# Kernel optimization log

Measured on AMD Instinct MI355X. Metric: run time of the kernel, lower is better.

The kernel has to match this reference:

```python
import jax, jax.numpy as jnp
import numpy as np

N, D, E, P, L = 50000, 128, 800000, 9, 3
EPS = 1e-5  # torch nn.LayerNorm default eps


def _layernorm(x, g, b):
    m = jnp.mean(x, axis=-1, keepdims=True)
    v = jnp.mean((x - m) ** 2, axis=-1, keepdims=True)
    return (x - m) * jax.lax.rsqrt(v + EPS) * g + b


def _pol_transform(x, M, onehot):
    # x: (N,d), M: (P,d,d), onehot: (N,P). Equivalent to bmm(x[n] @ M[pol[n]])
    # without materializing the (N,d,d) gathered map tensor.
    return jnp.einsum('nd,np,pdk->nk', x, onehot, M)


def setup_inputs() -> dict:
    key = jax.random.key(0)
    ks = jax.random.split(key, 12)
    s = 1.0 / np.sqrt(D)  # xavier-ish scale
    f32 = jnp.float32
    return {
        'x': jax.random.normal(ks[0], (N, D), f32),
        'edge_index': jax.random.randint(ks[1], (2, E), 0, N),
        'ring_polarities': jax.random.randint(ks[2], (N,), 0, P),
        'Wr': jax.random.normal(ks[3], (L, D, D), f32) * s,          # restriction weights
        'S': jax.random.normal(ks[4], (L, P, D, D), f32) * s,        # send_maps
        'dS': jax.random.normal(ks[5], (L, P, D, D), f32) * 0.01,    # delta_send
        'R': jax.random.normal(ks[6], (L, P, D, D), f32) * s,        # receive_maps
        'dR': jax.random.normal(ks[7], (L, P, D, D), f32) * 0.01,    # delta_receive
        'res_scale': jnp.full((L,), 0.92, f32),
        'W1': jax.random.normal(ks[8], (L, D, D), f32) * s,          # update Linear 1
        'b1': jnp.zeros((L, D), f32),
        'ln_g': jnp.ones((L, D), f32),                               # update LayerNorm
        'ln_b': jnp.zeros((L, D), f32),
        'W2': jax.random.normal(ks[9], (L, D, D), f32) * s,          # update Linear 2
        'b2': jnp.zeros((L, D), f32),
        'norm_g': jnp.ones((L, D), f32),                             # output LayerNorm
        'norm_b': jnp.zeros((L, D), f32),
    }


def reference(x, edge_index, ring_polarities, Wr, S, dS, R, dR, res_scale,
              W1, b1, ln_g, ln_b, W2, b2, norm_g, norm_b):
    src, tgt = edge_index[0], edge_index[1]
    pol = ring_polarities % P
    onehot = jax.nn.one_hot(pol, P, dtype=x.dtype)  # (N,P)
    # deg is accumulated over row(=src) in the original code, then used to
    # normalize the scatter over col(=tgt) -- preserved faithfully.
    deg = jax.ops.segment_sum(jnp.ones((E,), x.dtype), src, num_segments=N)
    deg_norm = (1.0 / jnp.clip(deg, 1.0))[:, None]  # (N,1)

    residual = x
    for l in range(L):
        # send transform: map depends only on src-node polarity, so apply
        # per-node then gather (algebraically identical to per-edge bmm).
        xt = _pol_transform(x, S[l] + dS[l], onehot)          # (N,D)
        msg = xt[src] @ Wr[l].T                               # (E,D) restriction per edge
        agg = jax.ops.segment_sum(msg, tgt, num_segments=N)   # index_add scatter
        # receive transform depends only on tgt polarity; linear, so it
        # commutes with the sum over incoming edges.
        out = _pol_transform(agg, R[l] + dR[l], onehot) * deg_norm
        # update MLP (dropout inactive in eval)
        h = jax.nn.relu(_layernorm(out @ W1[l].T + b1[l], ln_g[l], ln_b[l]))
        out = h @ W2[l].T + b2[l]
        out = res_scale[l] * out + x                           # in==out residual
        x = _layernorm(out, norm_g[l], norm_b[l])
    return x + residual  # stack-level residual (res_proj is None, dims match)
```

## Files before the change

kernel.cpp:

```cpp
#include <hip/hip_runtime.h>
#include <hip/hip_bf16.h>

constexpr int N_ = 50000;
constexpr int D_ = 128;
constexpr int E_ = 800000;
constexpr int P_ = 9;
constexpr int L_ = 3;
constexpr float EPS_ = 1e-5f;

constexpr int TM = 64;
constexpr int CHUNK = 4096;
constexpr int NBK = (E_ + CHUNK - 1) / CHUNK;
constexpr int NBUK = 196;
constexpr int HHALF = 256 * NBK;
constexpr int HTOT = 2 * HHALF;
constexpr int NSB = HTOT / 1024;
constexpr int MAT = L_ * P_;

typedef short bf16x8 __attribute__((ext_vector_type(8)));
typedef float f32x4 __attribute__((ext_vector_type(4)));

#define GLD16(gp, lp)                                                        \
    __builtin_amdgcn_global_load_lds(                                        \
        (const __attribute__((address_space(1))) unsigned int*)(gp),         \
        (__attribute__((address_space(3))) unsigned int*)(lp), 16, 0, 0)

__device__ inline unsigned short f2bf(float f) {
    __hip_bfloat16 h = __float2bfloat16(f);
    return *reinterpret_cast<unsigned short*>(&h);
}
__device__ inline float bflo(unsigned u) { return __uint_as_float(u << 16); }
__device__ inline float bfhi(unsigned u) { return __uint_as_float(u & 0xffff0000u); }
__device__ inline float bf2f(unsigned short h) {
    return __uint_as_float((unsigned)h << 16);
}


__global__ __launch_bounds__(256) void setup_nk(const int* __restrict__ ring,
                                                int* __restrict__ pol,
                                                int* __restrict__ bcnt,
                                                const int* __restrict__ ei,
                                                int* __restrict__ histG) {
    __shared__ int h[P_];
    __shared__ int hT[256], hS[256];
    int blk = blockIdx.x, tid = threadIdx.x;
    if (tid < P_) h[tid] = 0;
    hT[tid] = 0;
    hS[tid] = 0;
    __syncthreads();
    int n = blk * 256 + tid;
    if (n < N_) {
        int p = ring[n] % P_;
        pol[n] = p;
        atomicAdd(&h[p], 1);
    }
    int base = blk * CHUNK;
#pragma unroll
    for (int i = 0; i < CHUNK / 256; ++i) {
        int e = base + tid + i * 256;
        if (e < E_) {
            atomicAdd(&hS[ei[e] >> 8], 1);
            atomicAdd(&hT[ei[E_ + e] >> 8], 1);
        }
    }
    __syncthreads();
    if (tid < P_ && h[tid] > 0) atomicAdd(&bcnt[tid], h[tid]);
    histG[tid * NBK + blk] = hT[tid];
    histG[HHALF + tid * NBK + blk] = hS[tid];
}


__global__ __launch_bounds__(1024) void scanH1(int* __restrict__ a,
                                               int* __restrict__ blkSum) {
    __shared__ int wsum[16];
    int tid = threadIdx.x, lane = tid & 63, wid = tid >> 6;
    int idx = blockIdx.x * 1024 + tid;
    int v = a[idx];
    int inc = v;
#pragma unroll
    for (int o = 1; o < 64; o <<= 1) {
        int t = __shfl_up(inc, o, 64);
        if (lane >= o) inc += t;
    }
    if (lane == 63) wsum[wid] = inc;
    __syncthreads();
    if (tid < 16) {
        int s = wsum[tid];
#pragma unroll
        for (int o = 1; o < 16; o <<= 1) {
            int t = __shfl_up(s, o, 64);
            if (tid >= o) s += t;
        }
        wsum[tid] = s;
    }
    __syncthreads();
    int wexcl = (wid == 0) ? 0 : wsum[wid - 1];
    a[idx] = wexcl + inc - v;
    if (tid == 1023) blkSum[blockIdx.x] = wsum[15];
}

__global__ void scanH2(const int* __restrict__ blkSum, int* __restrict__ blkOff,
                       int* __restrict__ offT, const int* __restrict__ bcnt,
                       int* __restrict__ boff, int* __restrict__ tileOff) {
    if (threadIdx.x != 0) return;
    int run = 0;
    for (int i = 0; i < NSB; ++i) {
        blkOff[i] = run;
        run += blkSum[i];
    }
    offT[N_] = E_;
    boff[0] = 0;
    tileOff[0] = 0;
    for (int p = 0; p < P_; ++p) {
        boff[p + 1] = boff[p] + bcnt[p];
        tileOff[p + 1] = tileOff[p] + (bcnt[p] + TM - 1) / TM;
    }
}

__global__ __launch_bounds__(1024) void scanH3(int* __restrict__ a,
                                               const int* __restrict__ blkOff) {
    int idx = blockIdx.x * 1024 + threadIdx.x;
    a[idx] += blkOff[blockIdx.x];
}


__global__ __launch_bounds__(256) void scatterTS(const int* __restrict__ ei,
                                                 const int* __restrict__ histG,
                                                 unsigned* __restrict__ bufT,
                                                 unsigned char* __restrict__ bufS8) {
    __shared__ int ldsT[256], ldsS[256];
    int blk = blockIdx.x, tid = threadIdx.x;
    ldsT[tid] = histG[tid * NBK + blk];
    ldsS[tid] = histG[HHALF + tid * NBK + blk] - E_;
    __syncthreads();
    int base = blk * CHUNK;
#pragma unroll
    for (int i = 0; i < CHUNK / 256; ++i) {
        int e = base + tid + i * 256;
        if (e < E_) {
            int s = ei[e], t = ei[E_ + e];
            int pT = atomicAdd(&ldsT[t >> 8], 1);
            bufT[pT] = ((unsigned)t << 16) | (unsigned)s;
            int pS = atomicAdd(&ldsS[s >> 8], 1);
            bufS8[pS] = (unsigned char)(s & 255);
        }
    }
}


__global__ __launch_bounds__(256) void finalize3(
    const unsigned* __restrict__ bufT, const unsigned char* __restrict__ bufS8,
    const int* __restrict__ histG, int* __restrict__ offT,
    unsigned short* __restrict__ eSrc, float* __restrict__ dnorm,
    const int* __restrict__ pol, const int* __restrict__ boff,
    int* __restrict__ bcur, int* __restrict__ blist) {
    __shared__ int s0[256];
    __shared__ int s1[256];
    int bb = blockIdx.x, tid = threadIdx.x;

    if (bb < NBUK) {
        int b = bb;
        int start = histG[b * NBK];
        int end = histG[(b + 1) * NBK];
        s0[tid] = 0;
        __syncthreads();
        for (int i = start + tid; i < end; i += 256)
            atomicAdd(&s0[(bufT[i] >> 16) & 255], 1);
        __syncthreads();
        if (tid < 64) {
            int b0 = 4 * tid;
            int v0 = s0[b0], v1 = s0[b0 + 1], v2 = s0[b0 + 2], v3 = s0[b0 + 3];
            int lsum = v0 + v1 + v2 + v3;
            int inc = lsum;
#pragma unroll
            for (int o = 1; o < 64; o <<= 1) {
                int t = __shfl_up(inc, o, 64);
                if (tid >= o) inc += t;
            }
            int excl = inc - lsum;
            s1[b0] = excl;
            s1[b0 + 1] = excl + v0;
            s1[b0 + 2] = excl + v0 + v1;
            s1[b0 + 3] = excl + v0 + v1 + v2;
        }
        __syncthreads();
        int node = (b << 8) + tid;
        if (node < N_) offT[node] = start + s1[tid];
// ... 89 lines not shown
        } else if (idx < SZ2) {
            j = idx - SZ1;
            v = W1[j];
            oh = W1h; ol = W1l;
        } else {
            j = idx - SZ2;
            int l = j >> 14, rem = j & 16383;
            int d = rem >> 7, i = rem & 127;
            v = Wr[(l << 14) + i * 128 + d];
            oh = Wrth; ol = Wrtl;
        }
        unsigned short h = f2bf(v);
        oh[j] = h;
        ol[j] = f2bf(v - bf2f(h));
    }
}


template <bool APM, bool BPM, bool OUT_SPLIT>
__global__ __launch_bounds__(256) void small_mfma(
    const unsigned short* __restrict__ Ah, const unsigned short* __restrict__ Al,
    const unsigned short* __restrict__ Bh, const unsigned short* __restrict__ Bl,
    unsigned short* __restrict__ Oh, unsigned short* __restrict__ Ol) {
    __shared__ unsigned short stg[(OUT_SPLIT ? 2 : 1) * 64 * 136];
    int tid = threadIdx.x, b = blockIdx.x;
    int mat = b >> 1, rb = b & 1;
    int l = mat / P_;
    size_t aoff = (size_t)(APM ? mat : l) * 16384 + (size_t)rb * 8192;
    size_t boff = (size_t)(BPM ? mat : l) * 16384;
    const unsigned short* ahp = Ah + aoff;
    const unsigned short* alp = Al + aoff;
    const unsigned short* bhp = Bh + boff;
    const unsigned short* blp = Bl + boff;

    int lane = tid & 63, wave = tid >> 6;
    int n = lane & 15, q = lane >> 4;
    int wr = wave * 16;

    f32x4 acc[8];
#pragma unroll
    for (int t = 0; t < 8; ++t) acc[t] = (f32x4){0.f, 0.f, 0.f, 0.f};

    int arow = (wr + n) * 128;
#pragma unroll
    for (int kc = 0; kc < 4; ++kc) {
        int ko = kc * 32 + q * 8;
        bf16x8 avh = *(const bf16x8*)(ahp + arow + ko);
        bf16x8 avl = *(const bf16x8*)(alp + arow + ko);
#pragma unroll
        for (int t = 0; t < 8; ++t) {
            int brow = (t * 16 + n) * 128;
            bf16x8 bvh = *(const bf16x8*)(bhp + brow + ko);
            bf16x8 bvl = *(const bf16x8*)(blp + brow + ko);
            acc[t] = __builtin_amdgcn_mfma_f32_16x16x32_bf16(avh, bvh, acc[t], 0, 0, 0);
            acc[t] = __builtin_amdgcn_mfma_f32_16x16x32_bf16(avh, bvl, acc[t], 0, 0, 0);
            acc[t] = __builtin_amdgcn_mfma_f32_16x16x32_bf16(avl, bvh, acc[t], 0, 0, 0);
        }
    }
#pragma unroll
    for (int t = 0; t < 8; ++t)
#pragma unroll
        for (int r = 0; r < 4; ++r) {
            int row = wr + q * 4 + r;
            float v = acc[t][r];
            unsigned short h = f2bf(v);
            stg[row * 136 + t * 16 + n] = h;
            if constexpr (OUT_SPLIT)
                stg[64 * 136 + row * 136 + t * 16 + n] = f2bf(v - bf2f(h));
        }
    __syncthreads();
    size_t obase = (size_t)mat * 16384 + (size_t)rb * 8192;
#pragma unroll
    for (int i = 0; i < 4; ++i) {
        int c = tid + i * 256;
        int r = c >> 4, off = c & 15;
        *(uint4*)(Oh + obase + r * 128 + off * 8) =
            *(const uint4*)(stg + r * 136 + off * 8);
        if constexpr (OUT_SPLIT)
            *(uint4*)(Ol + obase + r * 128 + off * 8) =
                *(const uint4*)(stg + 64 * 136 + r * 136 + off * 8);
    }
}


__device__ inline void accum_row(float* acc, uint4 r) {
    acc[0] += bflo(r.x); acc[1] += bfhi(r.x);
    acc[2] += bflo(r.y); acc[3] += bfhi(r.y);
    acc[4] += bflo(r.z); acc[5] += bfhi(r.z);
    acc[6] += bflo(r.w); acc[7] += bfhi(r.w);
}

__global__ __launch_bounds__(256) void aggregate_bf(const unsigned short* __restrict__ xt,
                                                    const int* __restrict__ offT,
                                                    const unsigned short* __restrict__ eSrc,
                                                    unsigned short* __restrict__ agg) {
    int nd = blockIdx.x * 4 + (threadIdx.x >> 6);
    if (nd >= N_) return;
    int l = threadIdx.x & 63;
    int g = l >> 4, c16 = l & 15;
    int beg = offT[nd], end = offT[nd + 1];

    float acc[8];
#pragma unroll
    for (int k = 0; k < 8; ++k) acc[k] = 0.f;

    for (int base = beg; base < end; base += 64) {
        int cnt = min(64, end - base);
        int idxv = (l < cnt) ? (int)eSrc[base + l] : 0;
        int steps = (cnt + 3) >> 2;
        int j = 0;
        for (; j + 3 < steps; j += 4) {
            int e0 = 4 * j + g, e1 = e0 + 4, e2 = e0 + 8, e3 = e0 + 12;
            int i0 = __shfl(idxv, e0, 64);
            int i1 = __shfl(idxv, e1, 64);
            int i2 = __shfl(idxv, e2, 64);
            int i3 = __shfl(idxv, e3, 64);
            int r0 = (e0 < cnt) ? i0 : N_;
            int r1 = (e1 < cnt) ? i1 : N_;
            int r2 = (e2 < cnt) ? i2 : N_;
            int r3 = (e3 < cnt) ? i3 : N_;
            uint4 v0 = ((const uint4*)(xt + (size_t)r0 * D_))[c16];
            uint4 v1 = ((const uint4*)(xt + (size_t)r1 * D_))[c16];
            uint4 v2 = ((const uint4*)(xt + (size_t)r2 * D_))[c16];
            uint4 v3 = ((const uint4*)(xt + (size_t)r3 * D_))[c16];
            accum_row(acc, v0);
            accum_row(acc, v1);
            accum_row(acc, v2);
            accum_row(acc, v3);
        }
        for (; j < steps; ++j) {
            int e0 = 4 * j + g;
            int i0 = __shfl(idxv, e0, 64);
            int r0 = (e0 < cnt) ? i0 : N_;
            uint4 v0 = ((const uint4*)(xt + (size_t)r0 * D_))[c16];
            accum_row(acc, v0);
        }
    }
#pragma unroll
    for (int k = 0; k < 8; ++k) {
        acc[k] += __shfl_xor(acc[k], 16, 64);
        acc[k] += __shfl_xor(acc[k], 32, 64);
    }
    if (g == 0) {
        uint4 o;
        o.x = (unsigned)f2bf(acc[0]) | ((unsigned)f2bf(acc[1]) << 16);
        o.y = (unsigned)f2bf(acc[2]) | ((unsigned)f2bf(acc[3]) << 16);
        o.z = (unsigned)f2bf(acc[4]) | ((unsigned)f2bf(acc[5]) << 16);
        o.w = (unsigned)f2bf(acc[6]) | ((unsigned)f2bf(acc[7]) << 16);
        ((uint4*)(agg + (size_t)nd * D_))[c16] = o;
    }
}


__device__ inline void stage_B_async(const unsigned short* __restrict__ B,
                                     unsigned short* sB, int wave, int lane) {
    int rsub = lane >> 4, cl = lane & 15;
#pragma unroll
    for (int j = 0; j < 8; ++j) {
        int seg = wave * 8 + j;
        int row = seg * 4 + rsub;
        GLD16(B + row * 128 + ((cl ^ (row & 15)) << 3), sB + seg * 512);
    }
}

__device__ inline void stage_A_async(const unsigned short* __restrict__ A,
                                     const int* rid, unsigned short* sA,
                                     int wave, int lane) {
    int rsub = lane >> 4, cl = lane & 15;
#pragma unroll
    for (int j = 0; j < 4; ++j) {
        int seg = wave * 4 + j;
        int rloc = seg * 4 + rsub;
        int rw = rid[rloc];
        size_t grow = (rw >= 0) ? (size_t)rw : (size_t)N_;
        GLD16(A + grow * 128 + ((cl ^ (rloc & 15)) << 3), sA + seg * 512);
    }
}


__global__ __launch_bounds__(256) void gemm_xt0(
    const unsigned short* __restrict__ A, const unsigned short* __restrict__ Bw,
    unsigned short* __restrict__ OutB, const int* __restrict__ blist,
    const int* __restrict__ boff, const int* __restrict__ tileOff) {
    __shared__ unsigned short sB[128 * 128];
    __shared__ unsigned short sA[64 * 128];
    __shared__ int rid[TM];
    int tid = threadIdx.x, b = blockIdx.x;
    if (b >= tileOff[P_]) return;
    int pp = 0;
    while (pp < P_ - 1 && b >= tileOff[pp + 1]) ++pp;
    int tb = b - tileOff[pp];
    int cnt = boff[pp + 1] - boff[pp];
    int nrows = min(TM, cnt - tb * TM);
    int rowbase = boff[pp] + tb * TM;

    if (tid < TM)
        rid[tid] = (tid < nrows) ? blist[rowbase + tid] : -1;
    __syncthreads();

    int lane = tid & 63, wave = tid >> 6;
    stage_B_async(Bw + (size_t)pp * D_ * D_, sB, wave, lane);
    stage_A_async(A, rid, sA, wave, lane);
    __syncthreads();

    int n = lane & 15, q = lane >> 4, wr = wave * 16;

    f32x4 acc[8];
#pragma unroll
    for (int t = 0; t < 8; ++t) acc[t] = (f32x4){0.f, 0.f, 0.f, 0.f};
#pragma unroll
    for (int kc = 0; kc < 4; ++kc) {
        int cs = (((kc << 2) + q) ^ n) << 3;
        bf16x8 af = *(const bf16x8*)(sA + (wr + n) * 128 + cs);
#pragma unroll
        for (int t = 0; t < 8; ++t) {
            bf16x8 bf = *(const bf16x8*)(sB + (t * 16 + n) * 128 + cs);
            acc[t] = __builtin_amdgcn_mfma_f32_16x16x32_bf16(af, bf, acc[t], 0, 0, 0);
        }
    }
    __syncthreads();
#pragma unroll
    for (int t = 0; t < 8; ++t)
#pragma unroll
        for (int r = 0; r < 4; ++r) {
            int rl = q * 4 + r;
            int c = ((t * 16 + n) >> 3);
            sA[(wr + rl) * 128 + ((c ^ rl) << 3) + (n & 7)] = f2bf(acc[t][r]);
        }
    __syncthreads();
#pragma unroll
    for (int i = 0; i < 4; ++i) {
        int cth = tid + i * 256;
        int r = cth >> 4, cl = cth & 15;
        int row = rid[r];
        if (row >= 0)
            *(uint4*)(OutB + (size_t)row * D_ + (cl << 3)) =
                *(const uint4*)(sA + r * 128 + ((cl ^ (r & 15)) << 3));
    }
}


template <bool LAST>
__global__ __launch_bounds__(256) void fused_layer(
    const unsigned short* __restrict__ agg, const unsigned short* __restrict__ DmAll,
    const unsigned short* __restrict__ W2b, const unsigned short* __restrict__ SnAll,
    const int* __restrict__ blist, const int* __restrict__ boff,
    const int* __restrict__ tileOff, const float* __restrict__ dnorm,
    const float* __restrict__ b1v, const float* __restrict__ g1v,
    const float* __restrict__ e1v, const float* __restrict__ b2v,
    const float* __restrict__ g2v, const float* __restrict__ e2v,
    const float* __restrict__ rs_ptr, const float* __restrict__ xres,
    const float* __restrict__ x0add, float* __restrict__ OutF,
    unsigned short* __restrict__ OutXt) {
    __shared__ unsigned short sB[128 * 128];
    __shared__ unsigned short sA[64 * 128];
    __shared__ int rid[TM];
    __shared__ float dnRow[TM];

    int tid = threadIdx.x, b = blockIdx.x;
    if (b >= tileOff[P_]) return;
    int pp = 0;
    while (pp < P_ - 1 && b >= tileOff[pp + 1]) ++pp;
    int tb = b - tileOff[pp];
    int cnt = boff[pp + 1] - boff[pp];
    int nrows = min(TM, cnt - tb * TM);
    int rowbase = boff[pp] + tb * TM;

    if (tid < TM) {
        int r = (tid < nrows) ? blist[rowbase + tid] : -1;
        rid[tid] = r;
        dnRow[tid] = (r >= 0) ? dnorm[r] : 1.f;
    }
    __syncthreads();

    int lane = tid & 63, wave = tid >> 6;
    stage_B_async(DmAll + (size_t)pp * D_ * D_, sB, wave, lane);
    stage_A_async(agg, rid, sA, wave, lane);

    int n = lane & 15, q = lane >> 4, wr = wave * 16;

    int rowid[4];
    float dn4[4];
#pragma unroll
    for (int r = 0; r < 4; ++r) {
        int rr = wr + q * 4 + r;
        rowid[r] = rid[rr];
        dn4[r] = dnRow[rr];
    }

    float xr[8][4];
#pragma unroll
    for (int t = 0; t < 8; ++t) {
        int col = t * 16 + n;
#pragma unroll
        for (int r = 0; r < 4; ++r)
            xr[t][r] = (rowid[r] >= 0) ? xres[(size_t)rowid[r] * D_ + col] : 0.f;
    }
    __syncthreads();

    f32x4 acc[8];
#pragma unroll
    for (int t = 0; t < 8; ++t) acc[t] = (f32x4){0.f, 0.f, 0.f, 0.f};
#pragma unroll
    for (int kc = 0; kc < 4; ++kc) {
        int cs = (((kc << 2) + q) ^ n) << 3;
        bf16x8 af = *(const bf16x8*)(sA + (wr + n) * 128 + cs);
#pragma unroll
        for (int t = 0; t < 8; ++t) {
            bf16x8 bf = *(const bf16x8*)(sB + (t * 16 + n) * 128 + cs);
            acc[t] = __builtin_amdgcn_mfma_f32_16x16x32_bf16(af, bf, acc[t], 0, 0, 0);
        }
    }

    {
        float rs1[4] = {0, 0, 0, 0}, rs2[4] = {0, 0, 0, 0};
#pragma unroll
        for (int t = 0; t < 8; ++t) {
            int col = t * 16 + n;
            float bia = b1v[col];
#pragma unroll
            for (int r = 0; r < 4; ++r) {
                float v = dn4[r] * acc[t][r] + bia;
                acc[t][r] = v;
                rs1[r] += v;
                rs2[r] += v * v;
            }
        }
#pragma unroll
        for (int mk = 1; mk < 16; mk <<= 1)
#pragma unroll
            for (int r = 0; r < 4; ++r) {
                rs1[r] += __shfl_xor(rs1[r], mk, 64);
                rs2[r] += __shfl_xor(rs2[r], mk, 64);
            }
        float mr[4], rv[4];
#pragma unroll
        for (int r = 0; r < 4; ++r) {
            float mm = rs1[r] * (1.f / 128.f);
            mr[r] = mm;
            rv[r] = rsqrtf(rs2[r] * (1.f / 128.f) - mm * mm + EPS_);
        }
#pragma unroll
        for (int t = 0; t < 8; ++t) {
            int col = t * 16 + n;
            float gg = g1v[col], bbv = e1v[col];
#pragma unroll
            for (int r = 0; r < 4; ++r)
                acc[t][r] = fmaxf((acc[t][r] - mr[r]) * rv[r] * gg + bbv, 0.f);
        }
    }

    __syncthreads();
    stage_B_async(W2b, sB, wave, lane);
#pragma unroll
    for (int t = 0; t < 8; ++t)
#pragma unroll
        for (int r = 0; r < 4; ++r) {
            int rl = q * 4 + r;
            int c = ((t * 16 + n) >> 3);
            sA[(wr + rl) * 128 + ((c ^ rl) << 3) + (n & 7)] = f2bf(acc[t][r]);
        }
    __syncthreads();

#pragma unroll
    for (int t = 0; t < 8; ++t) acc[t] = (f32x4){0.f, 0.f, 0.f, 0.f};
#pragma unroll
    for (int kc = 0; kc < 4; ++kc) {
        int cs = (((kc << 2) + q) ^ n) << 3;
        bf16x8 af = *(const bf16x8*)(sA + (wr + n) * 128 + cs);
#pragma unroll
        for (int t = 0; t < 8; ++t) {
            bf16x8 bf = *(const bf16x8*)(sB + (t * 16 + n) * 128 + cs);
            acc[t] = __builtin_amdgcn_mfma_f32_16x16x32_bf16(af, bf, acc[t], 0, 0, 0);
        }
    }

    {
        float rs = rs_ptr[0];
        float rs1[4] = {0, 0, 0, 0}, rs2[4] = {0, 0, 0, 0};
#pragma unroll
        for (int t = 0; t < 8; ++t) {
            int col = t * 16 + n;
            float bia = b2v[col];
#pragma unroll
            for (int r = 0; r < 4; ++r) {
                float v = rs * (acc[t][r] + bia) + xr[t][r];
                acc[t][r] = v;
                rs1[r] += v;
                rs2[r] += v * v;
            }
        }
#pragma unroll
        for (int mk = 1; mk < 16; mk <<= 1)
#pragma unroll
            for (int r = 0; r < 4; ++r) {
                rs1[r] += __shfl_xor(rs1[r], mk, 64);
                rs2[r] += __shfl_xor(rs2[r], mk, 64);
            }
        float mr[4], rv[4];
#pragma unroll
        for (int r = 0; r < 4; ++r) {
            float mm = rs1[r] * (1.f / 128.f);
            mr[r] = mm;
            rv[r] = rsqrtf(rs2[r] * (1.f / 128.f) - mm * mm + EPS_);
        }
#pragma unroll
        for (int t = 0; t < 8; ++t) {
            int col = t * 16 + n;
            float gg = g2v[col], bbv = e2v[col];
#pragma unroll
            for (int r = 0; r < 4; ++r) {
                float nv = (acc[t][r] - mr[r]) * rv[r] * gg + bbv;
                if constexpr (LAST) {
                    if (rowid[r] >= 0) nv += x0add[(size_t)rowid[r] * D_ + col];
                }
                acc[t][r] = nv;
                if (rowid[r] >= 0) OutF[(size_t)rowid[r] * D_ + col] = nv;
            }
        }
    }

    if constexpr (!LAST) {
        __syncthreads();
        stage_B_async(SnAll + (size_t)pp * D_ * D_, sB, wave, lane);
#pragma unroll
        for (int t = 0; t < 8; ++t)
#pragma unroll
            for (int r = 0; r < 4; ++r) {
                int rl = q * 4 + r;
                int c = ((t * 16 + n) >> 3);
                sA[(wr + rl) * 128 + ((c ^ rl) << 3) + (n & 7)] = f2bf(acc[t][r]);
            }
        __syncthreads();

#pragma unroll
        for (int t = 0; t < 8; ++t) acc[t] = (f32x4){0.f, 0.f, 0.f, 0.f};
#pragma unroll
        for (int kc = 0; kc < 4; ++kc) {
            int cs = (((kc << 2) + q) ^ n) << 3;
            bf16x8 af = *(const bf16x8*)(sA + (wr + n) * 128 + cs);
#pragma unroll
            for (int t = 0; t < 8; ++t) {
                bf16x8 bf = *(const bf16x8*)(sB + (t * 16 + n) * 128 + cs);
                acc[t] = __builtin_amdgcn_mfma_f32_16x16x32_bf16(af, bf, acc[t], 0, 0, 0);
            }
        }
#pragma unroll
        for (int t = 0; t < 8; ++t)
#pragma unroll
            for (int r = 0; r < 4; ++r) {
                int rl = q * 4 + r;
                int c = ((t * 16 + n) >> 3);
                sA[(wr + rl) * 128 + ((c ^ rl) << 3) + (n & 7)] = f2bf(acc[t][r]);
            }
        __syncthreads();
#pragma unroll
        for (int i = 0; i < 4; ++i) {
            int cth = tid + i * 256;
            int r = cth >> 4, cl = cth & 15;
            int row = rid[r];
            if (row >= 0)
                *(uint4*)(OutXt + (size_t)row * D_ + (cl << 3)) =
                    *(const uint4*)(sA + r * 128 + ((cl ^ (r & 15)) << 3));
        }
    }
}


extern "C" void kernel_launch(void* const* d_in, const int* in_sizes, int n_in,
                              void* d_out, int out_size, void* d_ws, size_t ws_size,
                              hipStream_t stream) {
    const float* x0 = (const float*)d_in[0];
    const int* ei = (const int*)d_in[1];
    const int* ring = (const int*)d_in[2];
    const float* Wr = (const float*)d_in[3];
    const float* S = (const float*)d_in[4];
    const float* dS = (const float*)d_in[5];
    const float* R = (const float*)d_in[6];
    const float* dR = (const float*)d_in[7];
    const float* rsc = (const float*)d_in[8];
    const float* W1 = (const float*)d_in[9];
    const float* b1 = (const float*)d_in[10];
    const float* lng = (const float*)d_in[11];
    const float* lnb = (const float*)d_in[12];
    const float* W2 = (const float*)d_in[13];
    const float* b2 = (const float*)d_in[14];
    const float* ng = (const float*)d_in[15];
    const float* nb = (const float*)d_in[16];
    float* out = (float*)d_out;

    char* w = (char*)d_ws;
    auto alloc = [&](size_t bytes) {
        char* p = w;
        w += (bytes + 15) & ~(size_t)15;
        return p;
    };
    unsigned short* xb = (unsigned short*)alloc((size_t)(N_ + 1) * D_ * 2);
    unsigned short* bufAb = (unsigned short*)alloc((size_t)(N_ + 1) * D_ * 2);
    unsigned short* bufBb = (unsigned short*)alloc((size_t)(N_ + 1) * D_ * 2);
    float* xbuf = (float*)alloc((size_t)N_ * D_ * 4);
    unsigned short* Sb = (unsigned short*)alloc((size_t)L_ * P_ * D_ * D_ * 2);
    unsigned short* Dmb = (unsigned short*)alloc((size_t)L_ * P_ * D_ * D_ * 2);
    unsigned short* W2b = (unsigned short*)alloc((size_t)L_ * D_ * D_ * 2);
    unsigned short* Arh = (unsigned short*)alloc((size_t)MAT * 16384 * 2);
    unsigned short* Arl = (unsigned short*)alloc((size_t)MAT * 16384 * 2);
    unsigned short* W1h = (unsigned short*)alloc((size_t)3 * 16384 * 2);
    unsigned short* W1l = (unsigned short*)alloc((size_t)3 * 16384 * 2);
    unsigned short* Wrth = (unsigned short*)alloc((size_t)3 * 16384 * 2);
    unsigned short* Wrtl = (unsigned short*)alloc((size_t)3 * 16384 * 2);
    unsigned short* T1th = (unsigned short*)alloc((size_t)MAT * 16384 * 2);
    unsigned short* T1tl = (unsigned short*)alloc((size_t)MAT * 16384 * 2);
    float* dnorm = (float*)alloc((size_t)N_ * 4);
    int* histG = (int*)alloc((size_t)HTOT * 4);
    unsigned* bufT = (unsigned*)alloc((size_t)E_ * 4);
    unsigned char* bufS8 = (unsigned char*)alloc((size_t)E_);
    unsigned short* eSrc = (unsigned short*)alloc((size_t)E_ * 2);
    int* offT = (int*)alloc((size_t)(N_ + 1) * 4);
    int* pol = (int*)alloc((size_t)N_ * 4);
    int* boff = (int*)alloc((size_t)(P_ + 1) * 4);
    int* tileOff = (int*)alloc((size_t)(P_ + 1) * 4);
    int* blist = (int*)alloc((size_t)N_ * 4);
    int* blkSum = (int*)alloc((size_t)NSB * 4);
    int* blkOff = (int*)alloc((size_t)NSB * 4);
    int* bcnt = (int*)alloc((size_t)2 * P_ * 4);
    int* bcur = bcnt + P_;

    hipMemsetAsync(bcnt, 0, (size_t)2 * P_ * 4, stream);

    const int BTILES = N_ / TM + P_;

    setup_nk<<<NBK, 256, 0, stream>>>(ring, pol, bcnt, ei, histG);
    scanH1<<<NSB, 1024, 0, stream>>>(histG, blkSum);
    scanH2<<<1, 64, 0, stream>>>(blkSum, blkOff, offT, bcnt, boff, tileOff);
    scanH3<<<NSB, 1024, 0, stream>>>(histG, blkOff);
    scatterTS<<<NBK, 256, 0, stream>>>(ei, histG, bufT, bufS8);
    finalize3<<<3 * NBUK, 256, 0, stream>>>(bufT, bufS8, histG, offT, eSrc, dnorm,
                                            pol, boff, bcur, blist);
    prep_all<<<GPREP, 256, 0, stream>>>(x0, xb, bufAb, bufBb, S, dS, Sb, W2, W2b,
                                        R, dR, W1, Wr, Arh, Arl, W1h, W1l, Wrth, Wrtl);
    small_mfma<false, true, true><<<2 * MAT, 256, 0, stream>>>(
        W1h, W1l, Arh, Arl, T1th, T1tl);
    small_mfma<true, false, false><<<2 * MAT, 256, 0, stream>>>(
        T1th, T1tl, Wrth, Wrtl, Dmb, nullptr);

    gemm_xt0<<<BTILES, 256, 0, stream>>>(xb, Sb, bufAb, blist, boff, tileOff);

    for (int l = 0; l < L_; ++l) {
        const size_t lPDD = (size_t)l * P_ * D_ * D_;
        const size_t lDD = (size_t)l * D_ * D_;
        const size_t lD = (size_t)l * D_;
        aggregate_bf<<<N_ / 4, 256, 0, stream>>>(bufAb, offT, eSrc, bufBb);
        const float* xr = (l == 0) ? x0 : xbuf;
        if (l < L_ - 1) {
            fused_layer<false><<<BTILES, 256, 0, stream>>>(
                bufBb, Dmb + lPDD, W2b + lDD, Sb + lPDD + (size_t)P_ * D_ * D_,
                blist, boff, tileOff, dnorm,
                b1 + lD, lng + lD, lnb + lD, b2 + lD, ng + lD, nb + lD,
                rsc + l, xr, nullptr, xbuf, bufAb);
        } else {
            fused_layer<true><<<BTILES, 256, 0, stream>>>(
                bufBb, Dmb + lPDD, W2b + lDD, nullptr,
                blist, boff, tileOff, dnorm,
                b1 + lD, lng + lD, lnb + lD, b2 + lD, ng + lD, nb + lD,
                rsc + l, xr, x0, out, nullptr);
        }
    }
}
```

Baseline: 380.4 us.

## Read GEMM weights directly from global and make waves row-independent to drop barriers

Removes the 32KB LDS staging buffer for the 128x128 weight matrices in gemm_xt0 and fused_layer. MFMA B fragments are now loaded straight from global memory, relying on L1/L2 caching of the small per-polarity weights. Each wave now owns its 16 rows end to end (row ids, A staging, writeback), so most __syncthreads calls are removed. launch_bounds(256,4) is added, and the residual xres loads are deferred to where they are used to lower register pressure. The aim is higher occupancy and less barrier stalling, at the cost of repeated uncoalesced global/cache reads of the weights per wave.

```diff
diff --git a/kernel.cpp b/kernel.cpp
--- a/kernel.cpp
+++ b/kernel.cpp
@@ -428,17 +428,6 @@
 }
 
 
-__device__ inline void stage_B_async(const unsigned short* __restrict__ B,
-                                     unsigned short* sB, int wave, int lane) {
-    int rsub = lane >> 4, cl = lane & 15;
-#pragma unroll
-    for (int j = 0; j < 8; ++j) {
-        int seg = wave * 8 + j;
-        int row = seg * 4 + rsub;
-        GLD16(B + row * 128 + ((cl ^ (row & 15)) << 3), sB + seg * 512);
-    }
-}
-
 __device__ inline void stage_A_async(const unsigned short* __restrict__ A,
                                      const int* rid, unsigned short* sA,
                                      int wave, int lane) {
@@ -454,11 +443,10 @@
 }
 
 
-__global__ __launch_bounds__(256) void gemm_xt0(
+__global__ __launch_bounds__(256, 4) void gemm_xt0(
     const unsigned short* __restrict__ A, const unsigned short* __restrict__ Bw,
     unsigned short* __restrict__ OutB, const int* __restrict__ blist,
     const int* __restrict__ boff, const int* __restrict__ tileOff) {
-    __shared__ unsigned short sB[128 * 128];
     __shared__ unsigned short sA[64 * 128];
     __shared__ int rid[TM];
     int tid = threadIdx.x, b = blockIdx.x;
@@ -470,16 +458,16 @@
     int nrows = min(TM, cnt - tb * TM);
     int rowbase = boff[pp] + tb * TM;
 
-    if (tid < TM)
-        rid[tid] = (tid < nrows) ? blist[rowbase + tid] : -1;
+    int lane = tid & 63, wave = tid >> 6, wr = wave * 16;
+    if (lane < 16) {
+        int rr = wr + lane;
+        rid[rr] = (rr < nrows) ? blist[rowbase + rr] : -1;
+    }
+    stage_A_async(A, rid, sA, wave, lane);
+
+    const unsigned short* Bp = Bw + (size_t)pp * (D_ * D_);
+    int n = lane & 15, q = lane >> 4;
     __syncthreads();
-
-    int lane = tid & 63, wave = tid >> 6;
-    stage_B_async(Bw + (size_t)pp * D_ * D_, sB, wave, lane);
-    stage_A_async(A, rid, sA, wave, lane);
-    __syncthreads();
-
-    int n = lane & 15, q = lane >> 4, wr = wave * 16;
 
     f32x4 acc[8];
 #pragma unroll
@@ -488,13 +476,13 @@
     for (int kc = 0; kc < 4; ++kc) {
         int cs = (((kc << 2) + q) ^ n) << 3;
         bf16x8 af = *(const bf16x8*)(sA + (wr + n) * 128 + cs);
+        int ko = kc * 32 + q * 8;
 #pragma unroll
         for (int t = 0; t < 8; ++t) {
-            bf16x8 bf = *(const bf16x8*)(sB + (t * 16 + n) * 128 + cs);
+            bf16x8 bf = *(const bf16x8*)(Bp + (t * 16 + n) * 128 + ko);
             acc[t] = __builtin_amdgcn_mfma_f32_16x16x32_bf16(af, bf, acc[t], 0, 0, 0);
         }
     }
-    __syncthreads();
 #pragma unroll
     for (int t = 0; t < 8; ++t)
 #pragma unroll
@@ -503,21 +491,20 @@
             int c = ((t * 16 + n) >> 3);
             sA[(wr + rl) * 128 + ((c ^ rl) << 3) + (n & 7)] = f2bf(acc[t][r]);
         }
-    __syncthreads();
 #pragma unroll
     for (int i = 0; i < 4; ++i) {
-        int cth = tid + i * 256;
-        int r = cth >> 4, cl = cth & 15;
-        int row = rid[r];
+        int c = lane + i * 64;
+        int rl = c >> 4, cl = c & 15;
+        int row = rid[wr + rl];
         if (row >= 0)
             *(uint4*)(OutB + (size_t)row * D_ + (cl << 3)) =
-                *(const uint4*)(sA + r * 128 + ((cl ^ (r & 15)) << 3));
+                *(const uint4*)(sA + (wr + rl) * 128 + ((cl ^ rl) << 3));
     }
 }
 
 
 template <bool LAST>
-__global__ __launch_bounds__(256) void fused_layer(
+__global__ __launch_bounds__(256, 4) void fused_layer(
     const unsigned short* __restrict__ agg, const unsigned short* __restrict__ DmAll,
     const unsigned short* __restrict__ W2b, const unsigned short* __restrict__ SnAll,
     const int* __restrict__ blist, const int* __restrict__ boff,
@@ -528,7 +515,6 @@
     const float* __restrict__ rs_ptr, const float* __restrict__ xres,
     const float* __restrict__ x0add, float* __restrict__ OutF,
     unsigned short* __restrict__ OutXt) {
-    __shared__ unsigned short sB[128 * 128];
     __shared__ unsigned short sA[64 * 128];
     __shared__ int rid[TM];
     __shared__ float dnRow[TM];
@@ -542,19 +528,16 @@
     int nrows = min(TM, cnt - tb * TM);
     int rowbase = boff[pp] + tb * TM;
 
-    if (tid < TM) {
-        int r = (tid < nrows) ? blist[rowbase + tid] : -1;
-        rid[tid] = r;
-        dnRow[tid] = (r >= 0) ? dnorm[r] : 1.f;
-    }
-    __syncthreads();
-
-    int lane = tid & 63, wave = tid >> 6;
-    stage_B_async(DmAll + (size_t)pp * D_ * D_, sB, wave, lane);
+    int lane = tid & 63, wave = tid >> 6, wr = wave * 16;
+    if (lane < 16) {
+        int rr = wr + lane;
+        int r = (rr < nrows) ? blist[rowbase + rr] : -1;
+        rid[rr] = r;
+        dnRow[rr] = (r >= 0) ? dnorm[r] : 1.f;
+    }
     stage_A_async(agg, rid, sA, wave, lane);
 
-    int n = lane & 15, q = lane >> 4, wr = wave * 16;
-
+    int n = lane & 15, q = lane >> 4;
     int rowid[4];
     float dn4[4];
 #pragma unroll
@@ -563,15 +546,7 @@
         rowid[r] = rid[rr];
         dn4[r] = dnRow[rr];
     }
-
-    float xr[8][4];
-#pragma unroll
-    for (int t = 0; t < 8; ++t) {
-        int col = t * 16 + n;
-#pragma unroll
-        for (int r = 0; r < 4; ++r)
-            xr[t][r] = (rowid[r] >= 0) ? xres[(size_t)rowid[r] * D_ + col] : 0.f;
-    }
+    const unsigned short* Dmp = DmAll + (size_t)pp * (D_ * D_);
     __syncthreads();
 
     f32x4 acc[8];
@@ -581,9 +556,10 @@
     for (int kc = 0; kc < 4; ++kc) {
         int cs = (((kc << 2) + q) ^ n) << 3;
         bf16x8 af = *(const bf16x8*)(sA + (wr + n) * 128 + cs);
+        int ko = kc * 32 + q * 8;
 #pragma unroll
         for (int t = 0; t < 8; ++t) {
-            bf16x8 bf = *(const bf16x8*)(sB + (t * 16 + n) * 128 + cs);
+            bf16x8 bf = *(const bf16x8*)(Dmp + (t * 16 + n) * 128 + ko);
             acc[t] = __builtin_amdgcn_mfma_f32_16x16x32_bf16(af, bf, acc[t], 0, 0, 0);
         }
     }
@@ -626,8 +602,6 @@
         }
     }
 
-    __syncthreads();
-    stage_B_async(W2b, sB, wave, lane);
 #pragma unroll
     for (int t = 0; t < 8; ++t)
 #pragma unroll
@@ -636,7 +610,6 @@
             int c = ((t * 16 + n) >> 3);
             sA[(wr + rl) * 128 + ((c ^ rl) << 3) + (n & 7)] = f2bf(acc[t][r]);
         }
-    __syncthreads();
 
 #pragma unroll
     for (int t = 0; t < 8; ++t) acc[t] = (f32x4){0.f, 0.f, 0.f, 0.f};
@@ -644,9 +617,10 @@
     for (int kc = 0; kc < 4; ++kc) {
         int cs = (((kc << 2) + q) ^ n) << 3;
         bf16x8 af = *(const bf16x8*)(sA + (wr + n) * 128 + cs);
+        int ko = kc * 32 + q * 8;
 #pragma unroll
         for (int t = 0; t < 8; ++t) {
-            bf16x8 bf = *(const bf16x8*)(sB + (t * 16 + n) * 128 + cs);
+            bf16x8 bf = *(const bf16x8*)(W2b + (t * 16 + n) * 128 + ko);
             acc[t] = __builtin_amdgcn_mfma_f32_16x16x32_bf16(af, bf, acc[t], 0, 0, 0);
         }
     }
@@ -660,7 +634,8 @@
             float bia = b2v[col];
 #pragma unroll
             for (int r = 0; r < 4; ++r) {
-                float v = rs * (acc[t][r] + bia) + xr[t][r];
+                float xrv = (rowid[r] >= 0) ? xres[(size_t)rowid[r] * D_ + col] : 0.f;
+                float v = rs * (acc[t][r] + bia) + xrv;
                 acc[t][r] = v;
                 rs1[r] += v;
                 rs2[r] += v * v;
@@ -697,8 +672,7 @@
     }
 
     if constexpr (!LAST) {
-        __syncthreads();
-        stage_B_async(SnAll + (size_t)pp * D_ * D_, sB, wave, lane);
+        const unsigned short* Snp = SnAll + (size_t)pp * (D_ * D_);
 #pragma unroll
         for (int t = 0; t < 8; ++t)
 #pragma unroll
@@ -707,7 +681,6 @@
                 int c = ((t * 16 + n) >> 3);
                 sA[(wr + rl) * 128 + ((c ^ rl) << 3) + (n & 7)] = f2bf(acc[t][r]);
             }
-        __syncthreads();
 
 #pragma unroll
         for (int t = 0; t < 8; ++t) acc[t] = (f32x4){0.f, 0.f, 0.f, 0.f};
@@ -715,9 +688,10 @@
         for (int kc = 0; kc < 4; ++kc) {
             int cs = (((kc << 2) + q) ^ n) << 3;
             bf16x8 af = *(const bf16x8*)(sA + (wr + n) * 128 + cs);
+            int ko = kc * 32 + q * 8;
 #pragma unroll
             for (int t = 0; t < 8; ++t) {
-                bf16x8 bf = *(const bf16x8*)(sB + (t * 16 + n) * 128 + cs);
+                bf16x8 bf = *(const bf16x8*)(Snp + (t * 16 + n) * 128 + ko);
                 acc[t] = __builtin_amdgcn_mfma_f32_16x16x32_bf16(af, bf, acc[t], 0, 0, 0);
             }
         }
@@ -729,15 +703,14 @@
                 int c = ((t * 16 + n) >> 3);
                 sA[(wr + rl) * 128 + ((c ^ rl) << 3) + (n & 7)] = f2bf(acc[t][r]);
             }
-        __syncthreads();
 #pragma unroll
         for (int i = 0; i < 4; ++i) {
-            int cth = tid + i * 256;
-            int r = cth >> 4, cl = cth & 15;
-            int row = rid[r];
+            int c = lane + i * 64;
+            int rl = c >> 4, cl = c & 15;
+            int row = rid[wr + rl];
             if (row >= 0)
                 *(uint4*)(OutXt + (size_t)row * D_ + (cl << 3)) =
-                    *(const uint4*)(sA + r * 128 + ((cl ^ (r & 15)) << 3));
+                    *(const uint4*)(sA + (wr + rl) * 128 + ((cl ^ rl) << 3));
         }
     }
 }
```

Result: slower. 449.2 us (+18.1%).

## Swap MFMA operand roles to keep activations in registers, dropping sA staging

Applied to the files above, without the earlier changes.

The GEMMs in gemm_xt0 and fused_layer now use the weight tile from LDS as the A operand and the activation rows as the B operand, loaded straight from global memory into registers. This makes each lane own a whole row's outputs. LayerNorm reductions shrink to two cross-lane shuffles, outputs are written as vectorised row stores, and the intermediate activations are re-fragmented through lane shuffles instead of a round trip through LDS. Removing the sA buffer lowers shared memory use, and a launch bound of 4 blocks per CU is added to raise occupancy. The costs are higher register pressure and direct uncoalesced-ish gathers of activation rows.

```diff
diff --git a/kernel.cpp b/kernel.cpp
--- a/kernel.cpp
+++ b/kernel.cpp
@@ -33,6 +33,9 @@
 __device__ inline float bfhi(unsigned u) { return __uint_as_float(u & 0xffff0000u); }
 __device__ inline float bf2f(unsigned short h) {
     return __uint_as_float((unsigned)h << 16);
+}
+__device__ inline unsigned pack2bf(float a, float b) {
+    return (unsigned)f2bf(a) | ((unsigned)f2bf(b) << 16);
 }
 
 
@@ -439,28 +442,30 @@
     }
 }
 
-__device__ inline void stage_A_async(const unsigned short* __restrict__ A,
-                                     const int* rid, unsigned short* sA,
-                                     int wave, int lane) {
-    int rsub = lane >> 4, cl = lane & 15;
-#pragma unroll
-    for (int j = 0; j < 4; ++j) {
-        int seg = wave * 4 + j;
-        int rloc = seg * 4 + rsub;
-        int rw = rid[rloc];
-        size_t grow = (rw >= 0) ? (size_t)rw : (size_t)N_;
-        GLD16(A + grow * 128 + ((cl ^ (rloc & 15)) << 3), sA + seg * 512);
-    }
-}
-
-
-__global__ __launch_bounds__(256) void gemm_xt0(
+#define XCH_FRAG(dst, Pl, Ph, kc)                                            \
+    {                                                                        \
+        unsigned a0 = __shfl(Pl[2 * (kc)], s0, 64);                          \
+        unsigned b0 = __shfl(Pl[2 * (kc) + 1], s0, 64);                      \
+        unsigned a1 = __shfl(Ph[2 * (kc)], s0, 64);                          \
+        unsigned b1 = __shfl(Ph[2 * (kc) + 1], s0, 64);                      \
+        unsigned a2 = __shfl(Pl[2 * (kc)], s1, 64);                          \
+        unsigned b2 = __shfl(Pl[2 * (kc) + 1], s1, 64);                      \
+        unsigned a3 = __shfl(Ph[2 * (kc)], s1, 64);                          \
+        unsigned b3 = __shfl(Ph[2 * (kc) + 1], s1, 64);                      \
+        union { unsigned u[4]; bf16x8 v; } fu;                               \
+        fu.u[0] = hi ? b0 : a0;                                              \
+        fu.u[1] = hi ? b1 : a1;                                              \
+        fu.u[2] = hi ? b2 : a2;                                              \
+        fu.u[3] = hi ? b3 : a3;                                              \
+        dst = fu.v;                                                          \
+    }
+
+
+__global__ __launch_bounds__(256, 4) void gemm_xt0(
     const unsigned short* __restrict__ A, const unsigned short* __restrict__ Bw,
     unsigned short* __restrict__ OutB, const int* __restrict__ blist,
     const int* __restrict__ boff, const int* __restrict__ tileOff) {
     __shared__ unsigned short sB[128 * 128];
-    __shared__ unsigned short sA[64 * 128];
-    __shared__ int rid[TM];
     int tid = threadIdx.x, b = blockIdx.x;
     if (b >= tileOff[P_]) return;
     int pp = 0;
@@ -470,54 +475,45 @@
     int nrows = min(TM, cnt - tb * TM);
     int rowbase = boff[pp] + tb * TM;
 
-    if (tid < TM)
-        rid[tid] = (tid < nrows) ? blist[rowbase + tid] : -1;
-    __syncthreads();
-
     int lane = tid & 63, wave = tid >> 6;
-    stage_B_async(Bw + (size_t)pp * D_ * D_, sB, wave, lane);
-    stage_A_async(A, rid, sA, wave, lane);
-    __syncthreads();
-
-    int n = lane & 15, q = lane >> 4, wr = wave * 16;
+    int n = lane & 15, q = lane >> 4;
+    int rr = wave * 16 + n;
+    int rw = (rr < nrows) ? blist[rowbase + rr] : -1;
+    size_t grow = (rw >= 0) ? (size_t)rw : (size_t)N_;
+
+    stage_B_async(Bw + (size_t)pp * (D_ * D_), sB, wave, lane);
+    bf16x8 bg[4];
+#pragma unroll
+    for (int kc = 0; kc < 4; ++kc)
+        bg[kc] = *(const bf16x8*)(A + grow * 128 + kc * 32 + q * 8);
+    __syncthreads();
 
     f32x4 acc[8];
 #pragma unroll
     for (int t = 0; t < 8; ++t) acc[t] = (f32x4){0.f, 0.f, 0.f, 0.f};
 #pragma unroll
     for (int kc = 0; kc < 4; ++kc) {
-        int cs = (((kc << 2) + q) ^ n) << 3;
-        bf16x8 af = *(const bf16x8*)(sA + (wr + n) * 128 + cs);
 #pragma unroll
         for (int t = 0; t < 8; ++t) {
-            bf16x8 bf = *(const bf16x8*)(sB + (t * 16 + n) * 128 + cs);
-            acc[t] = __builtin_amdgcn_mfma_f32_16x16x32_bf16(af, bf, acc[t], 0, 0, 0);
-        }
-    }
-    __syncthreads();
-#pragma unroll
-    for (int t = 0; t < 8; ++t)
-#pragma unroll
-        for (int r = 0; r < 4; ++r) {
-            int rl = q * 4 + r;
-            int c = ((t * 16 + n) >> 3);
-            sA[(wr + rl) * 128 + ((c ^ rl) << 3) + (n & 7)] = f2bf(acc[t][r]);
-        }
-    __syncthreads();
-#pragma unroll
-    for (int i = 0; i < 4; ++i) {
-        int cth = tid + i * 256;
-        int r = cth >> 4, cl = cth & 15;
-        int row = rid[r];
-        if (row >= 0)
-            *(uint4*)(OutB + (size_t)row * D_ + (cl << 3)) =
-                *(const uint4*)(sA + r * 128 + ((cl ^ (r & 15)) << 3));
+            int cs = ((((kc << 2) + q) ^ n) << 3);
+            bf16x8 af = *(const bf16x8*)(sB + (t * 16 + n) * 128 + cs);
+            acc[t] = __builtin_amdgcn_mfma_f32_16x16x32_bf16(af, bg[kc], acc[t], 0, 0, 0);
+        }
+    }
+    if (rw >= 0) {
+#pragma unroll
+        for (int t = 0; t < 8; ++t) {
+            uint2 o;
+            o.x = pack2bf(acc[t][0], acc[t][1]);
+            o.y = pack2bf(acc[t][2], acc[t][3]);
+            *(uint2*)(OutB + (size_t)rw * 128 + t * 16 + q * 4) = o;
+        }
     }
 }
 
 
 template <bool LAST>
-__global__ __launch_bounds__(256) void fused_layer(
+__global__ __launch_bounds__(256, 4) void fused_layer(
     const unsigned short* __restrict__ agg, const unsigned short* __restrict__ DmAll,
     const unsigned short* __restrict__ W2b, const unsigned short* __restrict__ SnAll,
     const int* __restrict__ blist, const int* __restrict__ boff,
@@ -529,9 +525,6 @@
     const float* __restrict__ x0add, float* __restrict__ OutF,
     unsigned short* __restrict__ OutXt) {
     __shared__ unsigned short sB[128 * 128];
-    __shared__ unsigned short sA[64 * 128];
-    __shared__ int rid[TM];
-    __shared__ float dnRow[TM];
 
     int tid = threadIdx.x, b = blockIdx.x;
     if (b >= tileOff[P_]) return;
@@ -542,202 +535,177 @@
     int nrows = min(TM, cnt - tb * TM);
     int rowbase = boff[pp] + tb * TM;
 
-    if (tid < TM) {
-        int r = (tid < nrows) ? blist[rowbase + tid] : -1;
-        rid[tid] = r;
-        dnRow[tid] = (r >= 0) ? dnorm[r] : 1.f;
-    }
-    __syncthreads();
-
     int lane = tid & 63, wave = tid >> 6;
-    stage_B_async(DmAll + (size_t)pp * D_ * D_, sB, wave, lane);
-    stage_A_async(agg, rid, sA, wave, lane);
-
-    int n = lane & 15, q = lane >> 4, wr = wave * 16;
-
-    int rowid[4];
-    float dn4[4];
-#pragma unroll
-    for (int r = 0; r < 4; ++r) {
-        int rr = wr + q * 4 + r;
-        rowid[r] = rid[rr];
-        dn4[r] = dnRow[rr];
-    }
-
-    float xr[8][4];
+    int n = lane & 15, q = lane >> 4;
+    int rr = wave * 16 + n;
+    int rw = (rr < nrows) ? blist[rowbase + rr] : -1;
+    size_t grow = (rw >= 0) ? (size_t)rw : (size_t)N_;
+    int s0 = n + ((q & 1) << 5), s1 = s0 + 16;
+    bool hi = q >= 2;
+
+    stage_B_async(DmAll + (size_t)pp * (D_ * D_), sB, wave, lane);
+    bf16x8 bg[4];
+#pragma unroll
+    for (int kc = 0; kc < 4; ++kc)
+        bg[kc] = *(const bf16x8*)(agg + grow * 128 + kc * 32 + q * 8);
+    float dn = (rw >= 0) ? dnorm[rw] : 1.f;
+    __syncthreads();
+
+    f32x4 acc[8];
+#pragma unroll
+    for (int t = 0; t < 8; ++t) acc[t] = (f32x4){0.f, 0.f, 0.f, 0.f};
+#pragma unroll
+    for (int kc = 0; kc < 4; ++kc) {
+#pragma unroll
+        for (int t = 0; t < 8; ++t) {
+            int cs = ((((kc << 2) + q) ^ n) << 3);
+            bf16x8 af = *(const bf16x8*)(sB + (t * 16 + n) * 128 + cs);
+            acc[t] = __builtin_amdgcn_mfma_f32_16x16x32_bf16(af, bg[kc], acc[t], 0, 0, 0);
+        }
+    }
+
+    unsigned Pl[8], Ph[8];
+    {
+        float rs1 = 0.f, rs2 = 0.f;
+#pragma unroll
+        for (int t = 0; t < 8; ++t) {
+            float4 bb = *(const float4*)(b1v + t * 16 + q * 4);
+#pragma unroll
+            for (int r = 0; r < 4; ++r) {
+                float v = dn * acc[t][r] + (&bb.x)[r];
+                acc[t][r] = v;
+                rs1 += v;
+                rs2 += v * v;
+            }
+        }
+        rs1 += __shfl_xor(rs1, 16, 64);
+        rs1 += __shfl_xor(rs1, 32, 64);
+        rs2 += __shfl_xor(rs2, 16, 64);
+        rs2 += __shfl_xor(rs2, 32, 64);
+        float mm = rs1 * (1.f / 128.f);
+        float rv = rsqrtf(rs2 * (1.f / 128.f) - mm * mm + EPS_);
+#pragma unroll
+        for (int t = 0; t < 8; ++t) {
+            float4 gg = *(const float4*)(g1v + t * 16 + q * 4);
+            float4 ee = *(const float4*)(e1v + t * 16 + q * 4);
+            float h0 = fmaxf((acc[t][0] - mm) * rv * gg.x + ee.x, 0.f);
+            float h1 = fmaxf((acc[t][1] - mm) * rv * gg.y + ee.y, 0.f);
+            float h2 = fmaxf((acc[t][2] - mm) * rv * gg.z + ee.z, 0.f);
+            float h3 = fmaxf((acc[t][3] - mm) * rv * gg.w + ee.w, 0.f);
+            Pl[t] = pack2bf(h0, h1);
+            Ph[t] = pack2bf(h2, h3);
+        }
+    }
+
+    __syncthreads();
+    stage_B_async(W2b, sB, wave, lane);
+    bf16x8 h2[4];
+#pragma unroll
+    for (int kc = 0; kc < 4; ++kc) XCH_FRAG(h2[kc], Pl, Ph, kc)
+    float4 xrq[8];
 #pragma unroll
     for (int t = 0; t < 8; ++t) {
-        int col = t * 16 + n;
-#pragma unroll
-        for (int r = 0; r < 4; ++r)
-            xr[t][r] = (rowid[r] >= 0) ? xres[(size_t)rowid[r] * D_ + col] : 0.f;
-    }
-    __syncthreads();
-
-    f32x4 acc[8];
+        if (rw >= 0)
+            xrq[t] = *(const float4*)(xres + (size_t)rw * 128 + t * 16 + q * 4);
+        else
+            xrq[t] = float4{0.f, 0.f, 0.f, 0.f};
+    }
+    __syncthreads();
+
 #pragma unroll
     for (int t = 0; t < 8; ++t) acc[t] = (f32x4){0.f, 0.f, 0.f, 0.f};
 #pragma unroll
     for (int kc = 0; kc < 4; ++kc) {
-        int cs = (((kc << 2) + q) ^ n) << 3;
-        bf16x8 af = *(const bf16x8*)(sA + (wr + n) * 128 + cs);
 #pragma unroll
         for (int t = 0; t < 8; ++t) {
-            bf16x8 bf = *(const bf16x8*)(sB + (t * 16 + n) * 128 + cs);
-            acc[t] = __builtin_amdgcn_mfma_f32_16x16x32_bf16(af, bf, acc[t], 0, 0, 0);
-        }
-    }
-
+            int cs = ((((kc << 2) + q) ^ n) << 3);
+            bf16x8 af = *(const bf16x8*)(sB + (t * 16 + n) * 128 + cs);
+            acc[t] = __builtin_amdgcn_mfma_f32_16x16x32_bf16(af, h2[kc], acc[t], 0, 0, 0);
+        }
+    }
+
+    float rsc = rs_ptr[0];
     {
-        float rs1[4] = {0, 0, 0, 0}, rs2[4] = {0, 0, 0, 0};
+        float rs1 = 0.f, rs2 = 0.f;
 #pragma unroll
         for (int t = 0; t < 8; ++t) {
-            int col = t * 16 + n;
-            float bia = b1v[col];
+            float4 bb = *(const float4*)(b2v + t * 16 + q * 4);
 #pragma unroll
             for (int r = 0; r < 4; ++r) {
-                float v = dn4[r] * acc[t][r] + bia;
+                float v = rsc * (acc[t][r] + (&bb.x)[r]) + (&xrq[t].x)[r];
                 acc[t][r] = v;
-                rs1[r] += v;
-                rs2[r] += v * v;
+                rs1 += v;
+                rs2 += v * v;
             }
         }
-#pragma unroll
-        for (int mk = 1; mk < 16; mk <<= 1)
-#pragma unroll
-            for (int r = 0; r < 4; ++r) {
-                rs1[r] += __shfl_xor(rs1[r], mk, 64);
-                rs2[r] += __shfl_xor(rs2[r], mk, 64);
+        rs1 += __shfl_xor(rs1, 16, 64);
+        rs1 += __shfl_xor(rs1, 32, 64);
+        rs2 += __shfl_xor(rs2, 16, 64);
+        rs2 += __shfl_xor(rs2, 32, 64);
+        float mm = rs1 * (1.f / 128.f);
+        float rv = rsqrtf(rs2 * (1.f / 128.f) - mm * mm + EPS_);
+        if constexpr (LAST) {
+#pragma unroll
+            for (int t = 0; t < 8; ++t) {
+                float4 gg = *(const float4*)(g2v + t * 16 + q * 4);
+                float4 ee = *(const float4*)(e2v + t * 16 + q * 4);
+                if (rw >= 0) {
+                    float4 xa = *(const float4*)(x0add + (size_t)rw * 128 + t * 16 + q * 4);
+                    float4 o;
+                    o.x = (acc[t][0] - mm) * rv * gg.x + ee.x + xa.x;
+                    o.y = (acc[t][1] - mm) * rv * gg.y + ee.y + xa.y;
+                    o.z = (acc[t][2] - mm) * rv * gg.z + ee.z + xa.z;
+                    o.w = (acc[t][3] - mm) * rv * gg.w + ee.w + xa.w;
+                    *(float4*)(OutF + (size_t)rw * 128 + t * 16 + q * 4) = o;
+                }
             }
-        float mr[4], rv[4];
-#pragma unroll
-        for (int r = 0; r < 4; ++r) {
-            float mm = rs1[r] * (1.f / 128.f);
-            mr[r] = mm;
-            rv[r] = rsqrtf(rs2[r] * (1.f / 128.f) - mm * mm + EPS_);
-        }
-#pragma unroll
-        for (int t = 0; t < 8; ++t) {
-            int col = t * 16 + n;
-            float gg = g1v[col], bbv = e1v[col];
-#pragma unroll
-            for (int r = 0; r < 4; ++r)
-                acc[t][r] = fmaxf((acc[t][r] - mr[r]) * rv[r] * gg + bbv, 0.f);
-        }
-    }
-
-    __syncthreads();
-    stage_B_async(W2b, sB, wave, lane);
-#pragma unroll
-    for (int t = 0; t < 8; ++t)
-#pragma unroll
-        for (int r = 0; r < 4; ++r) {
-            int rl = q * 4 + r;
-            int c = ((t * 16 + n) >> 3);
-            sA[(wr + rl) * 128 + ((c ^ rl) << 3) + (n & 7)] = f2bf(acc[t][r]);
-        }
-    __syncthreads();
-
-#pragma unroll
-    for (int t = 0; t < 8; ++t) acc[t] = (f32x4){0.f, 0.f, 0.f, 0.f};
-#pragma unroll
-    for (int kc = 0; kc < 4; ++kc) {
-        int cs = (((kc << 2) + q) ^ n) << 3;
-        bf16x8 af = *(const bf16x8*)(sA + (wr + n) * 128 + cs);
-#pragma unroll
-        for (int t = 0; t < 8; ++t) {
-            bf16x8 bf = *(const bf16x8*)(sB + (t * 16 + n) * 128 + cs);
-            acc[t] = __builtin_amdgcn_mfma_f32_16x16x32_bf16(af, bf, acc[t], 0, 0, 0);
-        }
-    }
-
-    {
-        float rs = rs_ptr[0];
-        float rs1[4] = {0, 0, 0, 0}, rs2[4] = {0, 0, 0, 0};
-#pragma unroll
-        for (int t = 0; t < 8; ++t) {
-            int col = t * 16 + n;
-            float bia = b2v[col];
-#pragma unroll
-            for (int r = 0; r < 4; ++r) {
-                float v = rs * (acc[t][r] + bia) + xr[t][r];
-                acc[t][r] = v;
-                rs1[r] += v;
-                rs2[r] += v * v;
+        } else {
+#pragma unroll
+            for (int t = 0; t < 8; ++t) {
+                float4 gg = *(const float4*)(g2v + t * 16 + q * 4);
+                float4 ee = *(const float4*)(e2v + t * 16 + q * 4);
+                float4 o;
+                o.x = (acc[t][0] - mm) * rv * gg.x + ee.x;
+                o.y = (acc[t][1] - mm) * rv * gg.y + ee.y;
+                o.z = (acc[t][2] - mm) * rv * gg.z + ee.z;
+                o.w = (acc[t][3] - mm) * rv * gg.w + ee.w;
+                xrq[t] = o;
+                Pl[t] = pack2bf(o.x, o.y);
+                Ph[t] = pack2bf(o.z, o.w);
             }
         }
-#pragma unroll
-        for (int mk = 1; mk < 16; mk <<= 1)
-#pragma unroll
-            for (int r = 0; r < 4; ++r) {
-                rs1[r] += __shfl_xor(rs1[r], mk, 64);
-                rs2[r] += __shfl_xor(rs2[r], mk, 64);
+    }
+
+    if constexpr (!LAST) {
+        __syncthreads();
+        stage_B_async(SnAll + (size_t)pp * (D_ * D_), sB, wave, lane);
+        bf16x8 x2[4];
+#pragma unroll
+        for (int kc = 0; kc < 4; ++kc) XCH_FRAG(x2[kc], Pl, Ph, kc)
+        __syncthreads();
+
+#pragma unroll
+        for (int t = 0; t < 8; ++t) acc[t] = (f32x4){0.f, 0.f, 0.f, 0.f};
+#pragma unroll
+        for (int kc = 0; kc < 4; ++kc) {
+#pragma unroll
+            for (int t = 0; t < 8; ++t) {
+                int cs = ((((kc << 2) + q) ^ n) << 3);
+                bf16x8 af = *(const bf16x8*)(sB + (t * 16 + n) * 128 + cs);
+                acc[t] = __builtin_amdgcn_mfma_f32_16x16x32_bf16(af, x2[kc], acc[t], 0, 0, 0);
             }
-        float mr[4], rv[4];
-#pragma unroll
-        for (int r = 0; r < 4; ++r) {
-            float mm = rs1[r] * (1.f / 128.f);
-            mr[r] = mm;
-            rv[r] = rsqrtf(rs2[r] * (1.f / 128.f) - mm * mm + EPS_);
-        }
-#pragma unroll
-        for (int t = 0; t < 8; ++t) {
-            int col = t * 16 + n;
-            float gg = g2v[col], bbv = e2v[col];
-#pragma unroll
-            for (int r = 0; r < 4; ++r) {
-                float nv = (acc[t][r] - mr[r]) * rv[r] * gg + bbv;
-                if constexpr (LAST) {
-                    if (rowid[r] >= 0) nv += x0add[(size_t)rowid[r] * D_ + col];
-                }
-                acc[t][r] = nv;
-                if (rowid[r] >= 0) OutF[(size_t)rowid[r] * D_ + col] = nv;
+        }
+        if (rw >= 0) {
+#pragma unroll
+            for (int t = 0; t < 8; ++t) {
+                uint2 o;
+                o.x = pack2bf(acc[t][0], acc[t][1]);
+                o.y = pack2bf(acc[t][2], acc[t][3]);
+                *(uint2*)(OutXt + (size_t)rw * 128 + t * 16 + q * 4) = o;
             }
-        }
-    }
-
-    if constexpr (!LAST) {
-        __syncthreads();
-        stage_B_async(SnAll + (size_t)pp * D_ * D_, sB, wave, lane);
-#pragma unroll
-        for (int t = 0; t < 8; ++t)
-#pragma unroll
-            for (int r = 0; r < 4; ++r) {
-                int rl = q * 4 + r;
-                int c = ((t * 16 + n) >> 3);
-                sA[(wr + rl) * 128 + ((c ^ rl) << 3) + (n & 7)] = f2bf(acc[t][r]);
-            }
-        __syncthreads();
-
-#pragma unroll
-        for (int t = 0; t < 8; ++t) acc[t] = (f32x4){0.f, 0.f, 0.f, 0.f};
-#pragma unroll
-        for (int kc = 0; kc < 4; ++kc) {
-            int cs = (((kc << 2) + q) ^ n) << 3;
-            bf16x8 af = *(const bf16x8*)(sA + (wr + n) * 128 + cs);
-#pragma unroll
-            for (int t = 0; t < 8; ++t) {
-                bf16x8 bf = *(const bf16x8*)(sB + (t * 16 + n) * 128 + cs);
-                acc[t] = __builtin_amdgcn_mfma_f32_16x16x32_bf16(af, bf, acc[t], 0, 0, 0);
-            }
-        }
-#pragma unroll
-        for (int t = 0; t < 8; ++t)
-#pragma unroll
-            for (int r = 0; r < 4; ++r) {
-                int rl = q * 4 + r;
-                int c = ((t * 16 + n) >> 3);
-                sA[(wr + rl) * 128 + ((c ^ rl) << 3) + (n & 7)] = f2bf(acc[t][r]);
-            }
-        __syncthreads();
-#pragma unroll
-        for (int i = 0; i < 4; ++i) {
-            int cth = tid + i * 256;
-            int r = cth >> 4, cl = cth & 15;
-            int row = rid[r];
-            if (row >= 0)
-                *(uint4*)(OutXt + (size_t)row * D_ + (cl << 3)) =
-                    *(const uint4*)(sA + r * 128 + ((cl ^ (r & 15)) << 3));
+#pragma unroll
+            for (int t = 0; t < 8; ++t)
+                *(float4*)(OutF + (size_t)rw * 128 + t * 16 + q * 4) = xrq[t];
         }
     }
 }
```

New measurement: 385.7 us. No clear change (+1.4%).
